# Optimization experiments

Hardware: AMD Instinct MI355X
Metric: run time of the kernel (lower is better)

Reference implementation:

```python
import jax, jax.numpy as jnp
import numpy as np

B, S, D_MODEL, H = 4, 1024, 768, 12
DEPTH = D_MODEL // H  # 64


def setup_inputs() -> dict:
    key = jax.random.key(0)
    ks = jax.random.split(key, 11)
    sd = 1.0 / np.sqrt(D_MODEL)
    return {
        "q": jax.random.normal(ks[0], (B, S, D_MODEL), jnp.float32),
        "k": jax.random.normal(ks[1], (B, S, D_MODEL), jnp.float32),
        "v": jax.random.normal(ks[2], (B, S, D_MODEL), jnp.float32),
        # NOTE: source uses [Dense(depth)] * num_heads -> ONE shared layer per q/k/v
        "Wq": jax.random.normal(ks[3], (D_MODEL, DEPTH), jnp.float32) * sd,
        "bq": jnp.zeros((DEPTH,), jnp.float32),
        "Wk": jax.random.normal(ks[4], (D_MODEL, DEPTH), jnp.float32) * sd,
        "bk": jnp.zeros((DEPTH,), jnp.float32),
        "Wv": jax.random.normal(ks[5], (D_MODEL, DEPTH), jnp.float32) * sd,
        "bv": jnp.zeros((DEPTH,), jnp.float32),
        "Wc": jax.random.normal(ks[6], (D_MODEL, D_MODEL), jnp.float32) * sd,
        "bc": jnp.zeros((D_MODEL,), jnp.float32),
    }


def reference(q, k, v, Wq, bq, Wk, bk, Wv, bv, Wc, bc):
    # All heads share the same weights (list * num_heads aliasing in source),
    # so compute one head and replicate. Heads produce identical outputs.
    qh = q @ Wq + bq  # [B, S, depth]
    kh = k @ Wk + bk
    vh = v @ Wv + bv
    # Source bug reproduced: dk = tf.shape(k)[1] on [B,H,S,depth] == num_heads
    scale = 1.0 / jnp.sqrt(jnp.float32(H))
    scores = jnp.einsum('bqd,bkd->bqk', qh, kh) * scale  # [B, S, S]
    weights = jax.nn.softmax(scores, axis=-1)
    oh = jnp.einsum('bqk,bkd->bqd', weights, vh)  # [B, S, depth]
    # concat of H identical heads along feature dim -> tile
    concat = jnp.tile(oh, (1, 1, H))  # [B, S, d_model]
    output = concat @ Wc + bc
    attention_weights = jnp.broadcast_to(weights[:, None], (B, H, S, S))
    return (output, attention_weights)
```

## Files before the change

### kernel.cpp

```cpp
#include <hip/hip_runtime.h>
#include <math.h>

#define BB 4
#define SS 1024
#define DM 768
#define HH 12
#define DEPTH 64
#define QBLK 8
#define PROWS 16
#define NROWS (BB * SS)

#define LBAR() asm volatile("s_waitcnt lgkmcnt(0)\n\ts_barrier" ::: "memory")

typedef float vfloat4 __attribute__((ext_vector_type(4)));
typedef short bf16x8 __attribute__((ext_vector_type(8)));
typedef float f32x4 __attribute__((ext_vector_type(4)));

__device__ inline ushort f2bf(float x) {
    uint u = __float_as_uint(x);
    u += 0x7FFFu + ((u >> 16) & 1u);
    return (ushort)(u >> 16);
}

__global__ __launch_bounds__(256, 3) void proj_kernel(
    const float* __restrict__ q, const float* __restrict__ k, const float* __restrict__ v,
    const float* __restrict__ Wq, const float* __restrict__ bq,
    const float* __restrict__ Wk, const float* __restrict__ bk,
    const float* __restrict__ Wv, const float* __restrict__ bv,
    float* __restrict__ qh, ushort* __restrict__ khu, ushort* __restrict__ vhT)
{
    __shared__ __align__(16) float rows[PROWS][DM];
    __shared__ float resT[DEPTH][PROWS + 1];
    const int nrb  = NROWS / PROWS;
    const int m    = blockIdx.x / nrb;
    const int rb   = blockIdx.x % nrb;
    const int row0 = rb * PROWS;
    const int t    = threadIdx.x;

    const float* src  = (m == 0) ? q  : (m == 1) ? k  : v;
    const float* W    = (m == 0) ? Wq : (m == 1) ? Wk : Wv;
    const float* bias = (m == 0) ? bq : (m == 1) ? bk : bv;

    const float4* s4 = (const float4*)(src + (size_t)row0 * DM);
    float4* r4 = (float4*)&rows[0][0];
    for (int i = t; i < PROWS * DM / 4; i += 256) r4[i] = s4[i];
    __syncthreads();

    const int d  = t & 63;
    const int rg = t >> 6;
    const float* Wp = W + d;
    float a0 = bias[d], a1 = a0, a2 = a0, a3 = a0;
    #pragma unroll 8
    for (int i = 0; i < DM; i += 4) {
        const float wv0 = Wp[(size_t)(i + 0) * DEPTH];
        const float wv1 = Wp[(size_t)(i + 1) * DEPTH];
        const float wv2 = Wp[(size_t)(i + 2) * DEPTH];
        const float wv3 = Wp[(size_t)(i + 3) * DEPTH];
        const float4 r0 = *(const float4*)&rows[rg * 4 + 0][i];
        const float4 r1 = *(const float4*)&rows[rg * 4 + 1][i];
        const float4 r2 = *(const float4*)&rows[rg * 4 + 2][i];
        const float4 r3 = *(const float4*)&rows[rg * 4 + 3][i];
        a0 = fmaf(r0.x, wv0, a0); a0 = fmaf(r0.y, wv1, a0); a0 = fmaf(r0.z, wv2, a0); a0 = fmaf(r0.w, wv3, a0);
        a1 = fmaf(r1.x, wv0, a1); a1 = fmaf(r1.y, wv1, a1); a1 = fmaf(r1.z, wv2, a1); a1 = fmaf(r1.w, wv3, a1);
        a2 = fmaf(r2.x, wv0, a2); a2 = fmaf(r2.y, wv1, a2); a2 = fmaf(r2.z, wv2, a2); a2 = fmaf(r2.w, wv3, a2);
        a3 = fmaf(r3.x, wv0, a3); a3 = fmaf(r3.y, wv1, a3); a3 = fmaf(r3.z, wv2, a3); a3 = fmaf(r3.w, wv3, a3);
    }
    if (m == 2) {
        resT[d][rg * 4 + 0] = a0;
        resT[d][rg * 4 + 1] = a1;
        resT[d][rg * 4 + 2] = a2;
        resT[d][rg * 4 + 3] = a3;
        __syncthreads();
        #pragma unroll
        for (int e = t; e < DEPTH * PROWS; e += 256) {
            const int dd = e >> 4, rr = e & 15;
            vhT[(size_t)dd * NROWS + row0 + rr] = f2bf(resT[dd][rr]);
        }
    } else if (m == 1) {
        ushort* du = khu + (size_t)(row0 + rg * 4) * DEPTH + d;
        du[0] = f2bf(a0); du[DEPTH] = f2bf(a1); du[2 * DEPTH] = f2bf(a2); du[3 * DEPTH] = f2bf(a3);
    } else {
        float* dp = qh + (size_t)(row0 + rg * 4) * DEPTH + d;
        dp[0] = a0; dp[DEPTH] = a1; dp[2 * DEPTH] = a2; dp[3 * DEPTH] = a3;
    }
}

__global__ __launch_bounds__(256) void wcred_kernel(
    const float* __restrict__ Wc, float* __restrict__ Wr)
{
    int idx = blockIdx.x * 256 + threadIdx.x;
    if (idx >= DEPTH * DM) return;
    int d = idx / DM, j = idx % DM;
    float s = 0.f;
    #pragma unroll
    for (int h = 0; h < HH; ++h)
        s += Wc[(size_t)(h * DEPTH + d) * DM + j];
    Wr[idx] = s;
}

__global__ __launch_bounds__(512, 4) void attn_core(
    const float* __restrict__ qh, const ushort* __restrict__ khu, const ushort* __restrict__ vhT,
    const float* __restrict__ Wr, const float* __restrict__ bc,
    float* __restrict__ out, float* __restrict__ attn)
{
    __shared__ __align__(16) ushort qf[16 * 72];
    __shared__ __align__(16) ushort kvbuf[256 * 72];
    __shared__ __align__(16) ushort pf[16 * 1032];
    __shared__ float redmax[16 * 8];
    __shared__ float redsum[16 * 8];

    const int t = threadIdx.x, l = t & 63, wid = t >> 6;
    const int li = l & 15, g4 = l >> 4;
    const int blk = blockIdx.x, b = blk >> 7;
    const int q0 = (blk & 127) * QBLK;
    const int key = t >> 1, hf = t & 1;

    {
        const int qq = t >> 6, dd = t & 63;
        qf[qq * 72 + dd] = f2bf(qh[((size_t)b * SS + q0 + qq) * DEPTH + dd] * 0.28867513459481287f);
        for (int i = t; i < 8 * 72; i += 512) qf[8 * 72 + i] = 0;
        for (int i = t; i < 8 * 1032; i += 512) pf[8 * 1032 + i] = 0;
    }

    const ushort* khb = khu + (size_t)b * SS * DEPTH;
    const ushort* vtb = vhT + (size_t)b * SS;

    uint4 kr0, kr1, kr2, kr3;
    {
        const uint4* g = (const uint4*)(khb + (size_t)key * DEPTH + hf * 32);
        kr0 = g[0]; kr1 = g[1]; kr2 = g[2]; kr3 = g[3];
    }
    LBAR();

    const bf16x8 a0 = *(const bf16x8*)&qf[li * 72 + g4 * 8];
    const bf16x8 a1 = *(const bf16x8*)&qf[li * 72 + 32 + g4 * 8];

    f32x4 c[8];
    #pragma unroll
    for (int i = 0; i < 8; ++i) c[i] = (f32x4){0.f, 0.f, 0.f, 0.f};

    #pragma unroll
    for (int s = 0; s < 4; ++s) {
        if (s) LBAR();
        {
            uint4* d4 = (uint4*)&kvbuf[key * 72 + hf * 32];
            d4[0] = kr0; d4[1] = kr1; d4[2] = kr2; d4[3] = kr3;
        }
        if (s < 3) {
            const uint4* g = (const uint4*)(khb + (size_t)((s + 1) * 256 + key) * DEPTH + hf * 32);
            kr0 = g[0]; kr1 = g[1]; kr2 = g[2]; kr3 = g[3];
        }
        LBAR();
        __builtin_amdgcn_s_setprio(1);
        #pragma unroll
        for (int jj = 0; jj < 2; ++jj) {
            const int tl = wid + 8 * jj;
            const int ci = 2 * s + jj;
            const bf16x8 b0 = *(const bf16x8*)&kvbuf[(tl * 16 + li) * 72 + g4 * 8];
            const bf16x8 b1 = *(const bf16x8*)&kvbuf[(tl * 16 + li) * 72 + 32 + g4 * 8];
            c[ci] = __builtin_amdgcn_mfma_f32_16x16x32_bf16(a0, b0, c[ci], 0, 0, 0);
            c[ci] = __builtin_amdgcn_mfma_f32_16x16x32_bf16(a1, b1, c[ci], 0, 0, 0);
        }
        __builtin_amdgcn_s_setprio(0);
    }

    const int vrow = t >> 5;
    const int vcol = (t & 31) * 8;
    uint4 vp0, vp1, vp2, vp3;
    {
        vp0 = *(const uint4*)(vtb + (size_t)(0 * 16 + vrow) * NROWS + vcol);
        vp1 = *(const uint4*)(vtb + (size_t)(1 * 16 + vrow) * NROWS + vcol);
        vp2 = *(const uint4*)(vtb + (size_t)(2 * 16 + vrow) * NROWS + vcol);
        vp3 = *(const uint4*)(vtb + (size_t)(3 * 16 + vrow) * NROWS + vcol);
    }

    float mx[4], sm[4], inv[4];
    #pragma unroll
    for (int r = 0; r < 4; ++r) {
        float m_ = c[0][r];
        #pragma unroll
        for (int i = 1; i < 8; ++i) m_ = fmaxf(m_, c[i][r]);
        #pragma unroll
        for (int off = 1; off < 16; off <<= 1) m_ = fmaxf(m_, __shfl_xor(m_, off));
        mx[r] = m_;
    }
    if (li == 0) {
        #pragma unroll
        for (int r = 0; r < 4; ++r) redmax[(4 * g4 + r) * 8 + wid] = mx[r];
    }
    LBAR();
    #pragma unroll
    for (int r = 0; r < 4; ++r) {
        float m_ = redmax[(4 * g4 + r) * 8];
        #pragma unroll
        for (int w2 = 1; w2 < 8; ++w2) m_ = fmaxf(m_, redmax[(4 * g4 + r) * 8 + w2]);
        mx[r] = m_;
        sm[r] = 0.f;
    }
    #pragma unroll
    for (int i = 0; i < 8; ++i) {
        #pragma unroll
        for (int r = 0; r < 4; ++r) {
            const float e = __expf(c[i][r] - mx[r]);
            c[i][r] = e;
            sm[r] += e;
        }
    }
    #pragma unroll
    for (int r = 0; r < 4; ++r) {
        float s_ = sm[r];
        #pragma unroll
        for (int off = 1; off < 16; off <<= 1) s_ += __shfl_xor(s_, off);
        sm[r] = s_;
    }
    if (li == 0) {
        #pragma unroll
        for (int r = 0; r < 4; ++r) redsum[(4 * g4 + r) * 8 + wid] = sm[r];
    }
    LBAR();
    #pragma unroll
    for (int r = 0; r < 4; ++r) {
        float s_ = 0.f;
        #pragma unroll
        for (int w2 = 0; w2 < 8; ++w2) s_ += redsum[(4 * g4 + r) * 8 + w2];
        inv[r] = 1.f / s_;
    }
    if (l < 32) {
        #pragma unroll
        for (int i = 0; i < 8; ++i) {
            const int colbase = (16 * (i >> 1) + wid + 8 * (i & 1)) * 16 + li;
            #pragma unroll
            for (int r = 0; r < 4; ++r)
                pf[(4 * g4 + r) * 1032 + colbase] = f2bf(c[i][r] * inv[r]);
        }
    }
    LBAR();

    f32x4 cp = {0.f, 0.f, 0.f, 0.f};
    const int dt = wid >> 1, par = wid & 1;
    ushort* VT = kvbuf;
    #pragma unroll
    for (int s = 0; s < 4; ++s) {
        if (s) LBAR();
        {
            *(uint4*)&VT[(0 * 16 + vrow) * 264 + vcol] = vp0;
            *(uint4*)&VT[(1 * 16 + vrow) * 264 + vcol] = vp1;
            *(uint4*)&VT[(2 * 16 + vrow) * 264 + vcol] = vp2;
            *(uint4*)&VT[(3 * 16 + vrow) * 264 + vcol] = vp3;
        }
        if (s < 3) {
            const int sc = (s + 1) * 256;
            vp0 = *(const uint4*)(vtb + (size_t)(0 * 16 + vrow) * NROWS + sc + vcol);
            vp1 = *(const uint4*)(vtb + (size_t)(1 * 16 + vrow) * NROWS + sc + vcol);
            vp2 = *(const uint4*)(vtb + (size_t)(2 * 16 + vrow) * NROWS + sc + vcol);
            vp3 = *(const uint4*)(vtb + (size_t)(3 * 16 + vrow) * NROWS + sc + vcol);
        }
        LBAR();
        __builtin_amdgcn_s_setprio(1);
        #pragma unroll
        for (int c2 = 0; c2 < 4; ++c2) {
            const int cc = par + 2 * c2;
            const bf16x8 ap = *(const bf16x8*)&pf[li * 1032 + s * 256 + cc * 32 + g4 * 8];
            const bf16x8 bv = *(const bf16x8*)&VT[(dt * 16 + li) * 264 + cc * 32 + g4 * 8];
            cp = __builtin_amdgcn_mfma_f32_16x16x32_bf16(ap, bv, cp, 0, 0, 0);
        }
        __builtin_amdgcn_s_setprio(0);
    }
    LBAR();

    float* part_f = (float*)kvbuf;
    float* ohT_f  = ((float*)kvbuf) + 2048;
    #pragma unroll
    for (int r = 0; r < 4; ++r) part_f[wid * 256 + r * 64 + l] = cp[r];
    LBAR();
    {
        const int qq = t >> 6, dd = t & 63;
        const int ls = (qq >> 2) * 16 + (dd & 15), rr = qq & 3, w0 = (dd >> 4) * 2;
        ohT_f[dd * 12 + qq] = part_f[w0 * 256 + rr * 64 + ls] + part_f[(w0 + 1) * 256 + rr * 64 + ls];
    }
    LBAR();

    for (int j = t; j < DM; j += 512) {
        float a[QBLK];
        const float bj = bc[j];
        #pragma unroll
        for (int r = 0; r < QBLK; ++r) a[r] = bj;
        const float* wc = Wr + j;
        #pragma unroll 16
        for (int d2 = 0; d2 < DEPTH; ++d2) {
            const float wv = wc[(size_t)d2 * DM];
            const float4 o0 = *(const float4*)&ohT_f[d2 * 12];
            const float4 o1 = *(const float4*)&ohT_f[d2 * 12 + 4];
            a[0] = fmaf(o0.x, wv, a[0]); a[1] = fmaf(o0.y, wv, a[1]);
            a[2] = fmaf(o0.z, wv, a[2]); a[3] = fmaf(o0.w, wv, a[3]);
            a[4] = fmaf(o1.x, wv, a[4]); a[5] = fmaf(o1.y, wv, a[5]);
            a[6] = fmaf(o1.z, wv, a[6]); a[7] = fmaf(o1.w, wv, a[7]);
        }
        float* ob = out + ((size_t)b * SS + q0) * DM + j;
        #pragma unroll
        for (int r = 0; r < QBLK; ++r)
            __builtin_nontemporal_store(a[r], ob + (size_t)r * DM);
    }

    {
        const int qq = t >> 6, c0 = t & 63;
        const ushort* prow = &pf[qq * 1032];
        float* abase = attn + ((size_t)(b * HH) * SS + (q0 + qq)) * SS;
        #pragma unroll
        for (int i = 0; i < 4; ++i) {
            const int col = i * 256 + c0 * 4;
            vfloat4 v4;
            v4.x = __uint_as_float((uint)prow[col + 0] << 16);
            v4.y = __uint_as_float((uint)prow[col + 1] << 16);
            v4.z = __uint_as_float((uint)prow[col + 2] << 16);
            v4.w = __uint_as_float((uint)prow[col + 3] << 16);
            #pragma unroll
            for (int h = 0; h < HH; ++h)
                __builtin_nontemporal_store(v4, (vfloat4*)(abase + (size_t)h * SS * SS + col));
        }
    }
}

extern "C" void kernel_launch(void* const* d_in, const int* in_sizes, int n_in,
                              void* d_out, int out_size, void* d_ws, size_t ws_size,
                              hipStream_t stream) {
    const float* q  = (const float*)d_in[0];
    const float* k  = (const float*)d_in[1];
    const float* v  = (const float*)d_in[2];
    const float* Wq = (const float*)d_in[3];
    const float* bq = (const float*)d_in[4];
    const float* Wk = (const float*)d_in[5];
    const float* bk = (const float*)d_in[6];
    const float* Wv = (const float*)d_in[7];
    const float* bv = (const float*)d_in[8];
    const float* Wc = (const float*)d_in[9];
    const float* bc = (const float*)d_in[10];

    float* out  = (float*)d_out;
    float* attn = out + (size_t)BB * SS * DM;

    float* ws = (float*)d_ws;
    const size_t NPROJ = (size_t)NROWS * DEPTH;
    float* qh   = ws;
    ushort* khu = (ushort*)(ws + NPROJ);
    ushort* vhT = (ushort*)(ws + NPROJ + NPROJ / 2);
    float* Wr   = ws + 2 * NPROJ;

    wcred_kernel<<<(DEPTH * DM + 255) / 256, 256, 0, stream>>>(Wc, Wr);
    proj_kernel<<<3 * (NROWS / PROWS), 256, 0, stream>>>(q, k, v, Wq, bq, Wk, bk, Wv, bv, qh, khu, vhT);
    attn_core<<<BB * (SS / QBLK), 512, 0, stream>>>(qh, khu, vhT, Wr, bc, out, attn);
}
```

Before: 101.8 us.

## Add dedicated store waves to overlap attention-weight writes with PV compute

Grows the attention block from 512 to 768 threads and adds four wavefronts whose only job is writing the replicated attention-weight tensor. These waves skip the same number of block barriers as the compute waves up to the point where the probability tile is in LDS, then stream it out to all 12 heads. Meanwhile the compute waves continue with the PV matmul and the output projection. The aim is to hide the large, bandwidth-bound attention store behind the remaining compute. The cost is more waves per block, tighter register limits from the new launch bounds, and barrier counts that must stay hand-matched between the two wave groups.

```diff
diff --git a/kernel.cpp b/kernel.cpp
--- a/kernel.cpp
+++ b/kernel.cpp
@@ -98,7 +98,7 @@
     Wr[idx] = s;
 }
 
-__global__ __launch_bounds__(512, 4) void attn_core(
+__global__ __launch_bounds__(768, 6) void attn_core(
     const float* __restrict__ qh, const ushort* __restrict__ khu, const ushort* __restrict__ vhT,
     const float* __restrict__ Wr, const float* __restrict__ bc,
     float* __restrict__ out, float* __restrict__ attn)
@@ -110,214 +110,225 @@
     __shared__ float redsum[16 * 8];
 
     const int t = threadIdx.x, l = t & 63, wid = t >> 6;
-    const int li = l & 15, g4 = l >> 4;
     const int blk = blockIdx.x, b = blk >> 7;
     const int q0 = (blk & 127) * QBLK;
-    const int key = t >> 1, hf = t & 1;
-
-    {
-        const int qq = t >> 6, dd = t & 63;
-        qf[qq * 72 + dd] = f2bf(qh[((size_t)b * SS + q0 + qq) * DEPTH + dd] * 0.28867513459481287f);
-        for (int i = t; i < 8 * 72; i += 512) qf[8 * 72 + i] = 0;
-        for (int i = t; i < 8 * 1032; i += 512) pf[8 * 1032 + i] = 0;
-    }
-
-    const ushort* khb = khu + (size_t)b * SS * DEPTH;
-    const ushort* vtb = vhT + (size_t)b * SS;
-
-    uint4 kr0, kr1, kr2, kr3;
-    {
-        const uint4* g = (const uint4*)(khb + (size_t)key * DEPTH + hf * 32);
-        kr0 = g[0]; kr1 = g[1]; kr2 = g[2]; kr3 = g[3];
-    }
-    LBAR();
-
-    const bf16x8 a0 = *(const bf16x8*)&qf[li * 72 + g4 * 8];
-    const bf16x8 a1 = *(const bf16x8*)&qf[li * 72 + 32 + g4 * 8];
-
-    f32x4 c[8];
-    #pragma unroll
-    for (int i = 0; i < 8; ++i) c[i] = (f32x4){0.f, 0.f, 0.f, 0.f};
-
-    #pragma unroll
-    for (int s = 0; s < 4; ++s) {
-        if (s) LBAR();
+
+    if (wid < 8) {
+        const int li = l & 15, g4 = l >> 4;
+        const int key = t >> 1, hf = t & 1;
+
         {
-            uint4* d4 = (uint4*)&kvbuf[key * 72 + hf * 32];
-            d4[0] = kr0; d4[1] = kr1; d4[2] = kr2; d4[3] = kr3;
-        }
-        if (s < 3) {
-            const uint4* g = (const uint4*)(khb + (size_t)((s + 1) * 256 + key) * DEPTH + hf * 32);
+            const int qq = t >> 6, dd = t & 63;
+            qf[qq * 72 + dd] = f2bf(qh[((size_t)b * SS + q0 + qq) * DEPTH + dd] * 0.28867513459481287f);
+            for (int i = t; i < 8 * 72; i += 512) qf[8 * 72 + i] = 0;
+            for (int i = t; i < 8 * 1032; i += 512) pf[8 * 1032 + i] = 0;
+        }
+
+        const ushort* khb = khu + (size_t)b * SS * DEPTH;
+        const ushort* vtb = vhT + (size_t)b * SS;
+
+        uint4 kr0, kr1, kr2, kr3;
+        {
+            const uint4* g = (const uint4*)(khb + (size_t)key * DEPTH + hf * 32);
             kr0 = g[0]; kr1 = g[1]; kr2 = g[2]; kr3 = g[3];
         }
         LBAR();
-        __builtin_amdgcn_s_setprio(1);
-        #pragma unroll
-        for (int jj = 0; jj < 2; ++jj) {
-            const int tl = wid + 8 * jj;
-            const int ci = 2 * s + jj;
-            const bf16x8 b0 = *(const bf16x8*)&kvbuf[(tl * 16 + li) * 72 + g4 * 8];
-            const bf16x8 b1 = *(const bf16x8*)&kvbuf[(tl * 16 + li) * 72 + 32 + g4 * 8];
-            c[ci] = __builtin_amdgcn_mfma_f32_16x16x32_bf16(a0, b0, c[ci], 0, 0, 0);
-            c[ci] = __builtin_amdgcn_mfma_f32_16x16x32_bf16(a1, b1, c[ci], 0, 0, 0);
-        }
-        __builtin_amdgcn_s_setprio(0);
-    }
-
-    const int vrow = t >> 5;
-    const int vcol = (t & 31) * 8;
-    uint4 vp0, vp1, vp2, vp3;
-    {
-        vp0 = *(const uint4*)(vtb + (size_t)(0 * 16 + vrow) * NROWS + vcol);
-        vp1 = *(const uint4*)(vtb + (size_t)(1 * 16 + vrow) * NROWS + vcol);
-        vp2 = *(const uint4*)(vtb + (size_t)(2 * 16 + vrow) * NROWS + vcol);
-        vp3 = *(const uint4*)(vtb + (size_t)(3 * 16 + vrow) * NROWS + vcol);
-    }
-
-    float mx[4], sm[4], inv[4];
-    #pragma unroll
-    for (int r = 0; r < 4; ++r) {
-        float m_ = c[0][r];
-        #pragma unroll
-        for (int i = 1; i < 8; ++i) m_ = fmaxf(m_, c[i][r]);
-        #pragma unroll
-        for (int off = 1; off < 16; off <<= 1) m_ = fmaxf(m_, __shfl_xor(m_, off));
-        mx[r] = m_;
-    }
-    if (li == 0) {
-        #pragma unroll
-        for (int r = 0; r < 4; ++r) redmax[(4 * g4 + r) * 8 + wid] = mx[r];
-    }
-    LBAR();
-    #pragma unroll
-    for (int r = 0; r < 4; ++r) {
-        float m_ = redmax[(4 * g4 + r) * 8];
-        #pragma unroll
-        for (int w2 = 1; w2 < 8; ++w2) m_ = fmaxf(m_, redmax[(4 * g4 + r) * 8 + w2]);
-        mx[r] = m_;
-        sm[r] = 0.f;
-    }
-    #pragma unroll
-    for (int i = 0; i < 8; ++i) {
+
+        const bf16x8 a0 = *(const bf16x8*)&qf[li * 72 + g4 * 8];
+        const bf16x8 a1 = *(const bf16x8*)&qf[li * 72 + 32 + g4 * 8];
+
+        f32x4 c[8];
+        #pragma unroll
+        for (int i = 0; i < 8; ++i) c[i] = (f32x4){0.f, 0.f, 0.f, 0.f};
+
+        #pragma unroll
+        for (int s = 0; s < 4; ++s) {
+            if (s) LBAR();
+            {
+                uint4* d4 = (uint4*)&kvbuf[key * 72 + hf * 32];
+                d4[0] = kr0; d4[1] = kr1; d4[2] = kr2; d4[3] = kr3;
+            }
+            if (s < 3) {
+                const uint4* g = (const uint4*)(khb + (size_t)((s + 1) * 256 + key) * DEPTH + hf * 32);
+                kr0 = g[0]; kr1 = g[1]; kr2 = g[2]; kr3 = g[3];
+            }
+            LBAR();
+            __builtin_amdgcn_s_setprio(1);
+            #pragma unroll
+            for (int jj = 0; jj < 2; ++jj) {
+                const int tl = wid + 8 * jj;
+                const int ci = 2 * s + jj;
+                const bf16x8 b0 = *(const bf16x8*)&kvbuf[(tl * 16 + li) * 72 + g4 * 8];
+                const bf16x8 b1 = *(const bf16x8*)&kvbuf[(tl * 16 + li) * 72 + 32 + g4 * 8];
+                c[ci] = __builtin_amdgcn_mfma_f32_16x16x32_bf16(a0, b0, c[ci], 0, 0, 0);
+                c[ci] = __builtin_amdgcn_mfma_f32_16x16x32_bf16(a1, b1, c[ci], 0, 0, 0);
+            }
+            __builtin_amdgcn_s_setprio(0);
+        }
+
+        const int vrow = t >> 5;
+        const int vcol = (t & 31) * 8;
+        uint4 vp0, vp1, vp2, vp3;
+        {
+            vp0 = *(const uint4*)(vtb + (size_t)(0 * 16 + vrow) * NROWS + vcol);
+            vp1 = *(const uint4*)(vtb + (size_t)(1 * 16 + vrow) * NROWS + vcol);
+            vp2 = *(const uint4*)(vtb + (size_t)(2 * 16 + vrow) * NROWS + vcol);
+            vp3 = *(const uint4*)(vtb + (size_t)(3 * 16 + vrow) * NROWS + vcol);
+        }
+
+        float mx[4], sm[4], inv[4];
         #pragma unroll
         for (int r = 0; r < 4; ++r) {
-            const float e = __expf(c[i][r] - mx[r]);
-            c[i][r] = e;
-            sm[r] += e;
-        }
-    }
-    #pragma unroll
-    for (int r = 0; r < 4; ++r) {
-        float s_ = sm[r];
-        #pragma unroll
-        for (int off = 1; off < 16; off <<= 1) s_ += __shfl_xor(s_, off);
-        sm[r] = s_;
-    }
-    if (li == 0) {
-        #pragma unroll
-        for (int r = 0; r < 4; ++r) redsum[(4 * g4 + r) * 8 + wid] = sm[r];
-    }
-    LBAR();
-    #pragma unroll
-    for (int r = 0; r < 4; ++r) {
-        float s_ = 0.f;
-        #pragma unroll
-        for (int w2 = 0; w2 < 8; ++w2) s_ += redsum[(4 * g4 + r) * 8 + w2];
-        inv[r] = 1.f / s_;
-    }
-    if (l < 32) {
+            float m_ = c[0][r];
+            #pragma unroll
+            for (int i = 1; i < 8; ++i) m_ = fmaxf(m_, c[i][r]);
+            #pragma unroll
+            for (int off = 1; off < 16; off <<= 1) m_ = fmaxf(m_, __shfl_xor(m_, off));
+            mx[r] = m_;
+        }
+        if (li == 0) {
+            #pragma unroll
+            for (int r = 0; r < 4; ++r) redmax[(4 * g4 + r) * 8 + wid] = mx[r];
+        }
+        LBAR();
+        #pragma unroll
+        for (int r = 0; r < 4; ++r) {
+            float m_ = redmax[(4 * g4 + r) * 8];
+            #pragma unroll
+            for (int w2 = 1; w2 < 8; ++w2) m_ = fmaxf(m_, redmax[(4 * g4 + r) * 8 + w2]);
+            mx[r] = m_;
+            sm[r] = 0.f;
+        }
         #pragma unroll
         for (int i = 0; i < 8; ++i) {
-            const int colbase = (16 * (i >> 1) + wid + 8 * (i & 1)) * 16 + li;
-            #pragma unroll
-            for (int r = 0; r < 4; ++r)
-                pf[(4 * g4 + r) * 1032 + colbase] = f2bf(c[i][r] * inv[r]);
-        }
-    }
-    LBAR();
-
-    f32x4 cp = {0.f, 0.f, 0.f, 0.f};
-    const int dt = wid >> 1, par = wid & 1;
-    ushort* VT = kvbuf;
-    #pragma unroll
-    for (int s = 0; s < 4; ++s) {
-        if (s) LBAR();
+            #pragma unroll
+            for (int r = 0; r < 4; ++r) {
+                const float e = __expf(c[i][r] - mx[r]);
+                c[i][r] = e;
+                sm[r] += e;
+            }
+        }
+        #pragma unroll
+        for (int r = 0; r < 4; ++r) {
+            float s_ = sm[r];
+            #pragma unroll
+            for (int off = 1; off < 16; off <<= 1) s_ += __shfl_xor(s_, off);
+            sm[r] = s_;
+        }
+        if (li == 0) {
+            #pragma unroll
+            for (int r = 0; r < 4; ++r) redsum[(4 * g4 + r) * 8 + wid] = sm[r];
+        }
+        LBAR();
+        #pragma unroll
+        for (int r = 0; r < 4; ++r) {
+            float s_ = 0.f;
+            #pragma unroll
+            for (int w2 = 0; w2 < 8; ++w2) s_ += redsum[(4 * g4 + r) * 8 + w2];
+            inv[r] = 1.f / s_;
+        }
+        if (l < 32) {
+            #pragma unroll
+            for (int i = 0; i < 8; ++i) {
+                const int colbase = (16 * (i >> 1) + wid + 8 * (i & 1)) * 16 + li;
+                #pragma unroll
+                for (int r = 0; r < 4; ++r)
+                    pf[(4 * g4 + r) * 1032 + colbase] = f2bf(c[i][r] * inv[r]);
+            }
+        }
+        LBAR();
+
+        f32x4 cp = {0.f, 0.f, 0.f, 0.f};
+        const int dt = wid >> 1, par = wid & 1;
+        ushort* VT = kvbuf;
+        #pragma unroll
+        for (int s = 0; s < 4; ++s) {
+            if (s) LBAR();
+            {
+                *(uint4*)&VT[(0 * 16 + vrow) * 264 + vcol] = vp0;
+                *(uint4*)&VT[(1 * 16 + vrow) * 264 + vcol] = vp1;
+                *(uint4*)&VT[(2 * 16 + vrow) * 264 + vcol] = vp2;
+                *(uint4*)&VT[(3 * 16 + vrow) * 264 + vcol] = vp3;
+            }
+            if (s < 3) {
+                const int sc = (s + 1) * 256;
+                vp0 = *(const uint4*)(vtb + (size_t)(0 * 16 + vrow) * NROWS + sc + vcol);
+                vp1 = *(const uint4*)(vtb + (size_t)(1 * 16 + vrow) * NROWS + sc + vcol);
+                vp2 = *(const uint4*)(vtb + (size_t)(2 * 16 + vrow) * NROWS + sc + vcol);
+                vp3 = *(const uint4*)(vtb + (size_t)(3 * 16 + vrow) * NROWS + sc + vcol);
+            }
+            LBAR();
+            __builtin_amdgcn_s_setprio(1);
+            #pragma unroll
+            for (int c2 = 0; c2 < 4; ++c2) {
+                const int cc = par + 2 * c2;
+                const bf16x8 ap = *(const bf16x8*)&pf[li * 1032 + s * 256 + cc * 32 + g4 * 8];
+                const bf16x8 bv = *(const bf16x8*)&VT[(dt * 16 + li) * 264 + cc * 32 + g4 * 8];
+                cp = __builtin_amdgcn_mfma_f32_16x16x32_bf16(ap, bv, cp, 0, 0, 0);
+            }
+            __builtin_amdgcn_s_setprio(0);
+        }
+        LBAR();
+
+        float* part_f = (float*)kvbuf;
+        float* ohT_f  = ((float*)kvbuf) + 2048;
+        #pragma unroll
+        for (int r = 0; r < 4; ++r) part_f[wid * 256 + r * 64 + l] = cp[r];
+        LBAR();
         {
-            *(uint4*)&VT[(0 * 16 + vrow) * 264 + vcol] = vp0;
-            *(uint4*)&VT[(1 * 16 + vrow) * 264 + vcol] = vp1;
-            *(uint4*)&VT[(2 * 16 + vrow) * 264 + vcol] = vp2;
-            *(uint4*)&VT[(3 * 16 + vrow) * 264 + vcol] = vp3;
-        }
-        if (s < 3) {
-            const int sc = (s + 1) * 256;
-            vp0 = *(const uint4*)(vtb + (size_t)(0 * 16 + vrow) * NROWS + sc + vcol);
-            vp1 = *(const uint4*)(vtb + (size_t)(1 * 16 + vrow) * NROWS + sc + vcol);
-            vp2 = *(const uint4*)(vtb + (size_t)(2 * 16 + vrow) * NROWS + sc + vcol);
-            vp3 = *(const uint4*)(vtb + (size_t)(3 * 16 + vrow) * NROWS + sc + vcol);
-        }
-        LBAR();
-        __builtin_amdgcn_s_setprio(1);
-        #pragma unroll
-        for (int c2 = 0; c2 < 4; ++c2) {
-            const int cc = par + 2 * c2;
-            const bf16x8 ap = *(const bf16x8*)&pf[li * 1032 + s * 256 + cc * 32 + g4 * 8];
-            const bf16x8 bv = *(const bf16x8*)&VT[(dt * 16 + li) * 264 + cc * 32 + g4 * 8];
-            cp = __builtin_amdgcn_mfma_f32_16x16x32_bf16(ap, bv, cp, 0, 0, 0);
-        }
-        __builtin_amdgcn_s_setprio(0);
-    }
-    LBAR();
-
-    float* part_f = (float*)kvbuf;
-    float* ohT_f  = ((float*)kvbuf) + 2048;
-    #pragma unroll
-    for (int r = 0; r < 4; ++r) part_f[wid * 256 + r * 64 + l] = cp[r];
-    LBAR();
-    {
-        const int qq = t >> 6, dd = t & 63;
-        const int ls = (qq >> 2) * 16 + (dd & 15), rr = qq & 3, w0 = (dd >> 4) * 2;
-        ohT_f[dd * 12 + qq] = part_f[w0 * 256 + rr * 64 + ls] + part_f[(w0 + 1) * 256 + rr * 64 + ls];
-    }
-    LBAR();
-
-    for (int j = t; j < DM; j += 512) {
-        float a[QBLK];
-        const float bj = bc[j];
-        #pragma unroll
-        for (int r = 0; r < QBLK; ++r) a[r] = bj;
-        const float* wc = Wr + j;
-        #pragma unroll 16
-        for (int d2 = 0; d2 < DEPTH; ++d2) {
-            const float wv = wc[(size_t)d2 * DM];
-            const float4 o0 = *(const float4*)&ohT_f[d2 * 12];
-            const float4 o1 = *(const float4*)&ohT_f[d2 * 12 + 4];
-            a[0] = fmaf(o0.x, wv, a[0]); a[1] = fmaf(o0.y, wv, a[1]);
-            a[2] = fmaf(o0.z, wv, a[2]); a[3] = fmaf(o0.w, wv, a[3]);
-            a[4] = fmaf(o1.x, wv, a[4]); a[5] = fmaf(o1.y, wv, a[5]);
-            a[6] = fmaf(o1.z, wv, a[6]); a[7] = fmaf(o1.w, wv, a[7]);
-        }
-        float* ob = out + ((size_t)b * SS + q0) * DM + j;
-        #pragma unroll
-        for (int r = 0; r < QBLK; ++r)
-            __builtin_nontemporal_store(a[r], ob + (size_t)r * DM);
-    }
-
-    {
-        const int qq = t >> 6, c0 = t & 63;
-        const ushort* prow = &pf[qq * 1032];
-        float* abase = attn + ((size_t)(b * HH) * SS + (q0 + qq)) * SS;
-        #pragma unroll
-        for (int i = 0; i < 4; ++i) {
-            const int col = i * 256 + c0 * 4;
-            vfloat4 v4;
-            v4.x = __uint_as_float((uint)prow[col + 0] << 16);
-            v4.y = __uint_as_float((uint)prow[col + 1] << 16);
-            v4.z = __uint_as_float((uint)prow[col + 2] << 16);
-            v4.w = __uint_as_float((uint)prow[col + 3] << 16);
-            #pragma unroll
-            for (int h = 0; h < HH; ++h)
-                __builtin_nontemporal_store(v4, (vfloat4*)(abase + (size_t)h * SS * SS + col));
-        }
+            const int qq = t >> 6, dd = t & 63;
+            const int ls = (qq >> 2) * 16 + (dd & 15), rr = qq & 3, w0 = (dd >> 4) * 2;
+            ohT_f[dd * 12 + qq] = part_f[w0 * 256 + rr * 64 + ls] + part_f[(w0 + 1) * 256 + rr * 64 + ls];
+        }
+        LBAR();
+
+        for (int j = t; j < DM; j += 512) {
+            float a[QBLK];
+            const float bj = bc[j];
+            #pragma unroll
+            for (int r = 0; r < QBLK; ++r) a[r] = bj;
+            const float* wc = Wr + j;
+            #pragma unroll 16
+            for (int d2 = 0; d2 < DEPTH; ++d2) {
+                const float wv = wc[(size_t)d2 * DM];
+                const float4 o0 = *(const float4*)&ohT_f[d2 * 12];
+                const float4 o1 = *(const float4*)&ohT_f[d2 * 12 + 4];
+                a[0] = fmaf(o0.x, wv, a[0]); a[1] = fmaf(o0.y, wv, a[1]);
+                a[2] = fmaf(o0.z, wv, a[2]); a[3] = fmaf(o0.w, wv, a[3]);
+                a[4] = fmaf(o1.x, wv, a[4]); a[5] = fmaf(o1.y, wv, a[5]);
+                a[6] = fmaf(o1.z, wv, a[6]); a[7] = fmaf(o1.w, wv, a[7]);
+            }
+            float* ob = out + ((size_t)b * SS + q0) * DM + j;
+            #pragma unroll
+            for (int r = 0; r < QBLK; ++r)
+                __builtin_nontemporal_store(a[r], ob + (size_t)r * DM);
+        }
+    } else {
+        #pragma unroll
+        for (int i = 0; i < 11; ++i) LBAR();
+
+        const int ts = t - 512;
+        const int col = ts * 4;
+        vfloat4 v[8];
+        #pragma unroll
+        for (int qq = 0; qq < 8; ++qq) {
+            const ushort* prow = &pf[qq * 1032 + col];
+            v[qq].x = __uint_as_float((uint)prow[0] << 16);
+            v[qq].y = __uint_as_float((uint)prow[1] << 16);
+            v[qq].z = __uint_as_float((uint)prow[2] << 16);
+            v[qq].w = __uint_as_float((uint)prow[3] << 16);
+        }
+        float* abase = attn + ((size_t)(b * HH) * SS + q0) * SS + col;
+        #pragma unroll
+        for (int h = 0; h < HH; ++h) {
+            float* hp = abase + (size_t)h * SS * SS;
+            #pragma unroll
+            for (int qq = 0; qq < 8; ++qq)
+                __builtin_nontemporal_store(v[qq], (vfloat4*)(hp + (size_t)qq * SS));
+        }
+
+        #pragma unroll
+        for (int i = 0; i < 10; ++i) LBAR();
     }
 }
 
@@ -348,5 +359,5 @@
 
     wcred_kernel<<<(DEPTH * DM + 255) / 256, 256, 0, stream>>>(Wc, Wr);
     proj_kernel<<<3 * (NROWS / PROWS), 256, 0, stream>>>(q, k, v, Wq, bq, Wk, bk, Wv, bv, qh, khu, vhT);
-    attn_core<<<BB * (SS / QBLK), 512, 0, stream>>>(qh, khu, vhT, Wr, bc, out, attn);
-}
+    attn_core<<<BB * (SS / QBLK), 768, 0, stream>>>(qh, khu, vhT, Wr, bc, out, attn);
+}
```

Result: no change. 100.7 us (-1.1%).

## Stream K/V tiles via global_load_lds double buffering with XOR swizzle

Applied to the files above, without the earlier changes.

Replaces register-staged K and V tile loads with direct global-to-LDS loads (global_load_lds, 16 bytes per lane) into two 128-row ping-pong buffers. Each tile is prefetched two stages ahead and the stage boundary waits on vmcnt. An XOR swizzle replaces the padded LDS layout to avoid bank conflicts. The goal is to remove the VGPR round trip and LDS store instructions and to overlap loads with MFMA work, at the cost of more stages and more barriers (8 instead of 4 per phase).

```diff
diff --git a/kernel.cpp b/kernel.cpp
--- a/kernel.cpp
+++ b/kernel.cpp
@@ -11,10 +11,17 @@
 #define NROWS (BB * SS)
 
 #define LBAR() asm volatile("s_waitcnt lgkmcnt(0)\n\ts_barrier" ::: "memory")
+#define WAITV2() asm volatile("s_waitcnt vmcnt(2)" ::: "memory")
+#define WAITV0() asm volatile("s_waitcnt vmcnt(0)" ::: "memory")
 
 typedef float vfloat4 __attribute__((ext_vector_type(4)));
 typedef short bf16x8 __attribute__((ext_vector_type(8)));
 typedef float f32x4 __attribute__((ext_vector_type(4)));
+
+#define GLD16(g, l)                                                            \
+    __builtin_amdgcn_global_load_lds(                                          \
+        (const __attribute__((address_space(1))) void*)(g),                    \
+        (__attribute__((address_space(3))) void*)(l), 16, 0, 0)
 
 __device__ inline ushort f2bf(float x) {
     uint u = __float_as_uint(x);
@@ -104,7 +111,7 @@
     float* __restrict__ out, float* __restrict__ attn)
 {
     __shared__ __align__(16) ushort qf[16 * 72];
-    __shared__ __align__(16) ushort kvbuf[256 * 72];
+    __shared__ __align__(16) ushort kv[2][128 * 64];
     __shared__ __align__(16) ushort pf[16 * 1032];
     __shared__ float redmax[16 * 8];
     __shared__ float redsum[16 * 8];
@@ -113,7 +120,12 @@
     const int li = l & 15, g4 = l >> 4;
     const int blk = blockIdx.x, b = blk >> 7;
     const int q0 = (blk & 127) * QBLK;
-    const int key = t >> 1, hf = t & 1;
+
+    const ushort* khb = khu + (size_t)b * SS * DEPTH;
+    const ushort* vtb = vhT + (size_t)b * SS;
+
+    const int kr0 = t >> 3, kg = t & 7;
+    const int vd0 = t >> 4, vg = t & 15;
 
     {
         const int qq = t >> 6, dd = t & 63;
@@ -122,14 +134,22 @@
         for (int i = t; i < 8 * 1032; i += 512) pf[8 * 1032 + i] = 0;
     }
 
-    const ushort* khb = khu + (size_t)b * SS * DEPTH;
-    const ushort* vtb = vhT + (size_t)b * SS;
-
-    uint4 kr0, kr1, kr2, kr3;
-    {
-        const uint4* g = (const uint4*)(khb + (size_t)key * DEPTH + hf * 32);
-        kr0 = g[0]; kr1 = g[1]; kr2 = g[2]; kr3 = g[3];
-    }
+    auto ISSUE_K = [&](int s) {
+        const char* gb = (const char*)khb + (size_t)(s * 128) * 128;
+        char* lb = (char*)&kv[s & 1][0];
+        GLD16(gb + (size_t)kr0 * 128 + ((kg ^ (kr0 & 7)) << 4), lb + t * 16);
+        const int r1 = 64 + kr0;
+        GLD16(gb + (size_t)r1 * 128 + ((kg ^ (r1 & 7)) << 4), lb + 8192 + t * 16);
+    };
+    auto ISSUE_V = [&](int s) {
+        const char* gb = (const char*)vtb + (size_t)(s * 128) * 2;
+        char* lb = (char*)&kv[s & 1][0];
+        GLD16(gb + (size_t)vd0 * (NROWS * 2) + (((vg ^ (vd0 & 15)) << 4)), lb + t * 16);
+        const int d1 = 32 + vd0;
+        GLD16(gb + (size_t)d1 * (NROWS * 2) + (((vg ^ (d1 & 15)) << 4)), lb + 8192 + t * 16);
+    };
+
+    ISSUE_K(0); ISSUE_K(1);
     LBAR();
 
     const bf16x8 a0 = *(const bf16x8*)&qf[li * 72 + g4 * 8];
@@ -139,40 +159,27 @@
     #pragma unroll
     for (int i = 0; i < 8; ++i) c[i] = (f32x4){0.f, 0.f, 0.f, 0.f};
 
-    #pragma unroll
-    for (int s = 0; s < 4; ++s) {
-        if (s) LBAR();
-        {
-            uint4* d4 = (uint4*)&kvbuf[key * 72 + hf * 32];
-            d4[0] = kr0; d4[1] = kr1; d4[2] = kr2; d4[3] = kr3;
-        }
-        if (s < 3) {
-            const uint4* g = (const uint4*)(khb + (size_t)((s + 1) * 256 + key) * DEPTH + hf * 32);
-            kr0 = g[0]; kr1 = g[1]; kr2 = g[2]; kr3 = g[3];
-        }
+    const int krow = wid * 16 + li;
+    const int ksl0 = ((g4    ) ^ (krow & 7)) * 8;
+    const int ksl1 = ((4 + g4) ^ (krow & 7)) * 8;
+    #pragma unroll
+    for (int s = 0; s < 8; ++s) {
+        if (s == 7) { WAITV0(); } else { WAITV2(); }
         LBAR();
         __builtin_amdgcn_s_setprio(1);
-        #pragma unroll
-        for (int jj = 0; jj < 2; ++jj) {
-            const int tl = wid + 8 * jj;
-            const int ci = 2 * s + jj;
-            const bf16x8 b0 = *(const bf16x8*)&kvbuf[(tl * 16 + li) * 72 + g4 * 8];
-            const bf16x8 b1 = *(const bf16x8*)&kvbuf[(tl * 16 + li) * 72 + 32 + g4 * 8];
-            c[ci] = __builtin_amdgcn_mfma_f32_16x16x32_bf16(a0, b0, c[ci], 0, 0, 0);
-            c[ci] = __builtin_amdgcn_mfma_f32_16x16x32_bf16(a1, b1, c[ci], 0, 0, 0);
+        {
+            const ushort* kb = &kv[s & 1][0];
+            const bf16x8 b0 = *(const bf16x8*)&kb[krow * 64 + ksl0];
+            const bf16x8 b1 = *(const bf16x8*)&kb[krow * 64 + ksl1];
+            c[s] = __builtin_amdgcn_mfma_f32_16x16x32_bf16(a0, b0, c[s], 0, 0, 0);
+            c[s] = __builtin_amdgcn_mfma_f32_16x16x32_bf16(a1, b1, c[s], 0, 0, 0);
         }
         __builtin_amdgcn_s_setprio(0);
-    }
-
-    const int vrow = t >> 5;
-    const int vcol = (t & 31) * 8;
-    uint4 vp0, vp1, vp2, vp3;
-    {
-        vp0 = *(const uint4*)(vtb + (size_t)(0 * 16 + vrow) * NROWS + vcol);
-        vp1 = *(const uint4*)(vtb + (size_t)(1 * 16 + vrow) * NROWS + vcol);
-        vp2 = *(const uint4*)(vtb + (size_t)(2 * 16 + vrow) * NROWS + vcol);
-        vp3 = *(const uint4*)(vtb + (size_t)(3 * 16 + vrow) * NROWS + vcol);
-    }
+        LBAR();
+        if (s < 6) ISSUE_K(s + 2);
+    }
+
+    ISSUE_V(0); ISSUE_V(1);
 
     float mx[4], sm[4], inv[4];
     #pragma unroll
@@ -228,7 +235,7 @@
     if (l < 32) {
         #pragma unroll
         for (int i = 0; i < 8; ++i) {
-            const int colbase = (16 * (i >> 1) + wid + 8 * (i & 1)) * 16 + li;
+            const int colbase = (i * 8 + wid) * 16 + li;
             #pragma unroll
             for (int r = 0; r < 4; ++r)
                 pf[(4 * g4 + r) * 1032 + colbase] = f2bf(c[i][r] * inv[r]);
@@ -238,38 +245,29 @@
 
     f32x4 cp = {0.f, 0.f, 0.f, 0.f};
     const int dt = wid >> 1, par = wid & 1;
-    ushort* VT = kvbuf;
-    #pragma unroll
-    for (int s = 0; s < 4; ++s) {
-        if (s) LBAR();
-        {
-            *(uint4*)&VT[(0 * 16 + vrow) * 264 + vcol] = vp0;
-            *(uint4*)&VT[(1 * 16 + vrow) * 264 + vcol] = vp1;
-            *(uint4*)&VT[(2 * 16 + vrow) * 264 + vcol] = vp2;
-            *(uint4*)&VT[(3 * 16 + vrow) * 264 + vcol] = vp3;
-        }
-        if (s < 3) {
-            const int sc = (s + 1) * 256;
-            vp0 = *(const uint4*)(vtb + (size_t)(0 * 16 + vrow) * NROWS + sc + vcol);
-            vp1 = *(const uint4*)(vtb + (size_t)(1 * 16 + vrow) * NROWS + sc + vcol);
-            vp2 = *(const uint4*)(vtb + (size_t)(2 * 16 + vrow) * NROWS + sc + vcol);
-            vp3 = *(const uint4*)(vtb + (size_t)(3 * 16 + vrow) * NROWS + sc + vcol);
-        }
+    const int vrow = dt * 16 + li;
+    #pragma unroll
+    for (int s = 0; s < 8; ++s) {
+        if (s == 7) { WAITV0(); } else { WAITV2(); }
         LBAR();
         __builtin_amdgcn_s_setprio(1);
-        #pragma unroll
-        for (int c2 = 0; c2 < 4; ++c2) {
-            const int cc = par + 2 * c2;
-            const bf16x8 ap = *(const bf16x8*)&pf[li * 1032 + s * 256 + cc * 32 + g4 * 8];
-            const bf16x8 bv = *(const bf16x8*)&VT[(dt * 16 + li) * 264 + cc * 32 + g4 * 8];
-            cp = __builtin_amdgcn_mfma_f32_16x16x32_bf16(ap, bv, cp, 0, 0, 0);
+        {
+            const ushort* vb = &kv[s & 1][0];
+            #pragma unroll
+            for (int c2 = 0; c2 < 2; ++c2) {
+                const int cc = par * 2 + c2;
+                const bf16x8 ap = *(const bf16x8*)&pf[li * 1032 + s * 128 + cc * 32 + g4 * 8];
+                const bf16x8 bv = *(const bf16x8*)&vb[vrow * 128 + (((cc * 4 + g4) ^ li) * 8)];
+                cp = __builtin_amdgcn_mfma_f32_16x16x32_bf16(ap, bv, cp, 0, 0, 0);
+            }
         }
         __builtin_amdgcn_s_setprio(0);
-    }
-    LBAR();
-
-    float* part_f = (float*)kvbuf;
-    float* ohT_f  = ((float*)kvbuf) + 2048;
+        LBAR();
+        if (s < 6) ISSUE_V(s + 2);
+    }
+
+    float* part_f = (float*)&kv[0][0];
+    float* ohT_f  = ((float*)&kv[0][0]) + 2048;
     #pragma unroll
     for (int r = 0; r < 4; ++r) part_f[wid * 256 + r * 64 + l] = cp[r];
     LBAR();
```

Measured after the change: 104.1 us. +2.2%, slower.
